# Kernel optimization log

Hardware: AMD Instinct MI355X
Metric: run time of the kernel (lower is better)

Reference implementation:

```python
import jax, jax.numpy as jnp
import numpy as np

DIM = 1024
N_HEADS = 16
HEAD_DIM = DIM // N_HEADS


def setup_inputs() -> dict:
    key = jax.random.key(0)
    ks = jax.random.split(key, 5)
    x = jax.random.normal(ks[0], (2, 2048, DIM), dtype=jnp.float32)
    # nn.Linear-style init scale
    s = 1.0 / np.sqrt(DIM)
    W_qkv = jax.random.uniform(ks[1], (DIM, 3 * DIM), jnp.float32, -s, s)
    b_qkv = jax.random.uniform(ks[2], (3 * DIM,), jnp.float32, -s, s)
    W_proj = jax.random.uniform(ks[3], (DIM, DIM), jnp.float32, -s, s)
    b_proj = jax.random.uniform(ks[4], (DIM,), jnp.float32, -s, s)
    return {"x": x, "W_qkv": W_qkv, "b_qkv": b_qkv, "W_proj": W_proj, "b_proj": b_proj}


def reference(x, W_qkv, b_qkv, W_proj, b_proj):
    B, S, D = x.shape
    scale = HEAD_DIM ** -0.5
    qkv = x @ W_qkv + b_qkv                                   # [B,S,3D]
    qkv = qkv.reshape(B, S, 3, N_HEADS, HEAD_DIM)
    q = qkv[:, :, 0].transpose(0, 2, 1, 3)                    # [B,H,S,d]
    k = qkv[:, :, 1].transpose(0, 2, 1, 3)
    v = qkv[:, :, 2].transpose(0, 2, 1, 3)
    attn = jnp.einsum('bhqd,bhkd->bhqk', q, k) * scale        # [B,H,S,S]
    attn = jax.nn.softmax(attn, axis=-1)
    out = jnp.einsum('bhqk,bhkd->bhqd', attn, v)              # [B,H,S,d]
    out = out.transpose(0, 2, 1, 3).reshape(B, S, D)
    return out @ W_proj + b_proj
```

## Files before the change

### kernel.cpp

```cpp
#include <hip/hip_runtime.h>
#include <stdint.h>

typedef unsigned short u16;
typedef __attribute__((ext_vector_type(8))) short bf16x8;
typedef __attribute__((ext_vector_type(4))) float f32x4;
typedef __attribute__((ext_vector_type(16))) float f32x16;
typedef __attribute__((ext_vector_type(4))) u16 us4;
typedef __attribute__((ext_vector_type(8))) u16 us8;

__device__ __forceinline__ u16 f2bf(float f) {
  union { float f; unsigned u; } v; v.f = f;
  unsigned r = v.u + 0x7fffu + ((v.u >> 16) & 1u);
  return (u16)(r >> 16);
}

__device__ __forceinline__ float bf2f(u16 b) {
  union { float f; unsigned u; } v; v.u = ((unsigned)b) << 16;
  return v.f;
}

__device__ __forceinline__ unsigned cvtpk(float a, float b) {
  unsigned r;
  asm("v_cvt_pk_bf16_f32 %0, %1, %2" : "=v"(r) : "v"(a), "v"(b));
  return r;
}

__device__ __forceinline__ float fast_exp2(float x) {
#if __has_builtin(__builtin_amdgcn_exp2f)
  return __builtin_amdgcn_exp2f(x);
#else
  return exp2f(x);
#endif
}

__device__ __forceinline__ void gld16(const void* g, void* l) {
  __builtin_amdgcn_global_load_lds(
      (const __attribute__((address_space(1))) void*)g,
      (__attribute__((address_space(3))) void*)l, 16, 0, 0);
}

__global__ void prep_kernel(const float* __restrict__ x, u16* __restrict__ Xb,
                            const float* __restrict__ Wqkv, u16* __restrict__ Wqkt,
                            const float* __restrict__ Wproj, u16* __restrict__ Wpt) {
  __shared__ u16 tile[32][33];
  const int blk = blockIdx.x;
  if (blk < 4096) {
    const int i = blk * 256 + threadIdx.x;
    f32x4 v = ((const f32x4*)x)[i];
    us4 r;
#pragma unroll
    for (int j = 0; j < 4; ++j) r[j] = f2bf(v[j]);
    ((us4*)Xb)[i] = r;
    return;
  }
  const float* in;
  u16* out;
  int R, C, t;
  if (blk < 7168) { in = Wqkv; out = Wqkt; R = 1024; C = 3072; t = blk - 4096; }
  else            { in = Wproj; out = Wpt; R = 1024; C = 1024; t = blk - 7168; }
  const int gx = (C == 3072) ? (t % 96) : (t % 32);
  const int gy = (C == 3072) ? (t / 96) : (t / 32);
  const int tx = threadIdx.x & 31, ty = threadIdx.x >> 5;
  const int c0 = gx * 32, r0 = gy * 32;
#pragma unroll
  for (int j = 0; j < 4; ++j)
    tile[ty + j * 8][tx] = f2bf(in[(size_t)(r0 + ty + j * 8) * C + c0 + tx]);
  __syncthreads();
#pragma unroll
  for (int j = 0; j < 4; ++j)
    out[(size_t)(c0 + ty + j * 8) * R + r0 + tx] = tile[tx][ty + j * 8];
}

__global__ __launch_bounds__(256) void qkv_gemm_kernel(
    const u16* __restrict__ A, const u16* __restrict__ Bt, const float* __restrict__ bias,
    u16* __restrict__ Qb, u16* __restrict__ Kb, u16* __restrict__ Vtb) {
  __shared__ u16 sm[17408];
  u16* As = sm;
  u16* Bs = sm + 4096;
  const int tid = threadIdx.x;
  const int w = tid >> 6, l = tid & 63, quad = l >> 4, lanelo = l & 15;
  const int wr = w >> 1, wc = w & 1;
  const int flat = blockIdx.x + 32 * blockIdx.y;
  const int xcd = flat & 7, lid = flat >> 3;
  const long m0 = (long)((xcd >> 1) * 8 + (lid & 7)) * 128;
  const long n0 = (long)((xcd & 1) * 12 + (lid >> 3)) * 128;

  f32x4 acc[4][4];
#pragma unroll
  for (int i = 0; i < 4; ++i)
#pragma unroll
    for (int j = 0; j < 4; ++j) acc[i][j] = (f32x4){0.f, 0.f, 0.f, 0.f};

  const u16* ag = A + (m0 + w * 32 + (l >> 2)) * 1024 + (l & 3) * 8;
  const u16* bg = Bt + (n0 + w * 32 + (l >> 2)) * 1024 + (l & 3) * 8;
  u16* asl = As + w * 1024;
  u16* bsl = Bs + w * 1024;

  for (int kt = 0; kt < 32; ++kt) {
    const int ko = kt * 32;
    gld16(ag + ko, asl);
    gld16(ag + 16 * 1024 + ko, asl + 512);
    gld16(bg + ko, bsl);
    gld16(bg + 16 * 1024 + ko, bsl + 512);
    __syncthreads();
    bf16x8 af[4], bf[4];
#pragma unroll
    for (int mt = 0; mt < 4; ++mt)
      af[mt] = *(const bf16x8*)(As + (wr * 64 + mt * 16 + lanelo) * 32 + quad * 8);
#pragma unroll
    for (int nt = 0; nt < 4; ++nt)
      bf[nt] = *(const bf16x8*)(Bs + (wc * 64 + nt * 16 + lanelo) * 32 + quad * 8);
#pragma unroll
    for (int mt = 0; mt < 4; ++mt)
#pragma unroll
      for (int nt = 0; nt < 4; ++nt)
        acc[mt][nt] = __builtin_amdgcn_mfma_f32_16x16x32_bf16(af[mt], bf[nt], acc[mt][nt], 0, 0, 0);
    __syncthreads();
  }

  const int t = (int)(n0 >> 10);
  const float scl = (t == 0) ? 0.18033688011112042f : 1.0f;

  float bias_v[4];
#pragma unroll
  for (int nt = 0; nt < 4; ++nt) bias_v[nt] = bias[n0 + wc * 64 + nt * 16 + lanelo];

  u16* Ct = sm;
#pragma unroll
  for (int mt = 0; mt < 4; ++mt)
#pragma unroll
    for (int nt = 0; nt < 4; ++nt)
#pragma unroll
      for (int r = 0; r < 4; ++r)
        Ct[(wr * 64 + mt * 16 + quad * 4 + r) * 136 + wc * 64 + nt * 16 + lanelo] =
            f2bf((acc[mt][nt][r] + bias_v[nt]) * scl);
  __syncthreads();

  const int b = (int)(m0 >> 11);
  const int s0 = (int)(m0 & 2047);
  const int h0 = (int)((n0 & 1023) >> 6);

  if (t < 2) {
    u16* dst = (t == 0) ? Qb : Kb;
#pragma unroll
    for (int p = 0; p < 8; ++p) {
      const int hh = p >> 2;
      const int sl = (p & 3) * 32 + (tid >> 3);
      const int c8 = tid & 7;
      us8 v = *(const us8*)(Ct + sl * 136 + hh * 64 + c8 * 8);
      const int pos = (c8 + sl) & 7;
      const size_t off = ((size_t)((b * 16 + h0 + hh) * 2048 + s0 + sl)) * 64 + pos * 8;
      *(us8*)(dst + off) = v;
    }
  } else {
#pragma unroll
    for (int p = 0; p < 8; ++p) {
      const int hh = p >> 2;
      const int dl = (p & 3) * 16 + (tid >> 4);
      const int c16 = tid & 15;
      us8 v;
#pragma unroll
      for (int j = 0; j < 8; ++j) v[j] = Ct[(c16 * 8 + j) * 136 + hh * 64 + dl];
      const int pos = (c16 + dl) & 15;
      const size_t off = ((size_t)((b * 16 + h0 + hh) * 64 + dl)) * 2048 + s0 + pos * 8;
      *(us8*)(Vtb + off) = v;
    }
  }
}

__global__ __launch_bounds__(512, 4) void attn_kernel(
    const u16* __restrict__ Qb, const u16* __restrict__ Kb,
    const u16* __restrict__ Vtb, u16* __restrict__ Ob) {
  __shared__ u16 Ks[2][2][4096];
  __shared__ u16 Vs[2][2][4096];
  const int tid = threadIdx.x;
  const int w8 = tid >> 6;
  const int z = w8 >> 2, w = w8 & 3;
  const int l = tid & 63;
  const int m = l & 31, hi = l >> 5;
  const int fid = blockIdx.x;
  const int head = (fid & 7) + 8 * ((fid >> 3) & 3);
  const int qt = fid >> 5;
  const u16* Qh = Qb + (size_t)head * 2048 * 64;
  const u16* Kh = Kb + (size_t)head * 2048 * 64;
  const u16* Vh = Vtb + (size_t)head * 64 * 2048;
  const int permaddr = (l ^ 32) << 2;

  const int qrow = qt * 128 + w * 32 + m;
  bf16x8 qf[4];
#pragma unroll
  for (int ks = 0; ks < 4; ++ks) {
    const int pos = (ks * 2 + hi + qrow) & 7;
    qf[ks] = *(const bf16x8*)(Qh + (size_t)qrow * 64 + pos * 8);
  }

  f32x16 o0, o1;
#pragma unroll
  for (int i = 0; i < 16; ++i) { o0[i] = 0.f; o1[i] = 0.f; }
  float sp[4] = {0.f, 0.f, 0.f, 0.f};

  auto stage = [&](int kb, int buf) {
    const u16* kbase = Kh + (size_t)kb * 4096;
#pragma unroll
    for (int j = 0; j < 2; ++j) {
      const int i = w * 2 + j;
      gld16(kbase + i * 512 + l * 8, &Ks[z][buf][i * 512]);
    }
    const int panel = kb >> 1, half = kb & 1;
#pragma unroll
    for (int j = 0; j < 2; ++j) {
      const int i = w * 2 + j;
      const int dd = i * 8 + (l >> 3);
      const int p = l & 7;
      const int q = (p - dd) & 7;
      const int pos16 = (half * 8 + q + dd) & 15;
      gld16(Vh + (size_t)dd * 2048 + panel * 128 + pos16 * 8,
            &Vs[z][buf][i * 512]);
    }
  };

  int cur = 0;
  stage(z * 16, 0);

  for (int kt = 0; kt < 16; ++kt) {
    __builtin_amdgcn_s_barrier();
    if (kt < 15) {
      stage(z * 16 + kt + 1, cur ^ 1);
      asm volatile("s_waitcnt vmcnt(4)" ::: "memory");
    } else {
      asm volatile("s_waitcnt vmcnt(0)" ::: "memory");
    }
    __builtin_amdgcn_s_barrier();

#pragma unroll
    for (int g = 0; g < 2; ++g) {
      f32x16 st;
#pragma unroll
      for (int i = 0; i < 16; ++i) st[i] = 0.f;
      const int key = g * 32 + m;
#pragma unroll
      for (int ks = 0; ks < 4; ++ks) {
        const int pos = (ks * 2 + hi + key) & 7;
        bf16x8 kf = *(const bf16x8*)(&Ks[z][cur][key * 64 + pos * 8]);
        st = __builtin_amdgcn_mfma_f32_32x32x16_bf16(kf, qf[ks], st, 0, 0, 0);
      }

      float p[16];
#pragma unroll
      for (int r = 0; r < 16; ++r) p[r] = fast_exp2(st[r]);
#pragma unroll
      for (int r = 0; r < 16; ++r) sp[r & 3] += p[r];

      unsigned W[8];
#pragma unroll
      for (int i = 0; i < 8; ++i) W[i] = cvtpk(p[2 * i], p[2 * i + 1]);

#pragma unroll
      for (int s = 0; s < 2; ++s) {
        unsigned w0 = W[4 * s], w1 = W[4 * s + 1];
        unsigned w2 = W[4 * s + 2], w3 = W[4 * s + 3];
        asm("v_permlane32_swap_b32 %0, %1" : "+v"(w0), "+v"(w2));
        asm("v_permlane32_swap_b32 %0, %1" : "+v"(w1), "+v"(w3));
        int4 fd;
        fd.x = (int)w0;
        fd.y = (int)w1;
        fd.z = (int)w2;
        fd.w = (int)w3;
        union { int4 i; bf16x8 v; } pu; pu.i = fd;
        const int c = g * 4 + s * 2 + hi;
#pragma unroll
        for (int n = 0; n < 2; ++n) {
          const int d = n * 32 + m;
          const int pos = (c + d) & 7;
          bf16x8 vf = *(const bf16x8*)(&Vs[z][cur][d * 64 + pos * 8]);
          if (n == 0) o0 = __builtin_amdgcn_mfma_f32_32x32x16_bf16(pu.v, vf, o0, 0, 0, 0);
          else        o1 = __builtin_amdgcn_mfma_f32_32x32x16_bf16(pu.v, vf, o1, 0, 0, 0);
        }
      }
    }
    cur ^= 1;
  }
  __syncthreads();

  const float sacc = (sp[0] + sp[1]) + (sp[2] + sp[3]);

  union { float f; int i; } sv; sv.f = sacc;
  union { float f; int i; } pv; pv.i = __builtin_amdgcn_ds_bpermute(permaddr, sv.i);
  const float ltot = sacc + pv.f;

  float* Osl = (float*)Ks;
  float* Lz1 = (float*)Vs;

  if (z == 1) {
    if (hi == 0) Lz1[w * 32 + m] = ltot;
#pragma unroll
    for (int r = 0; r < 16; ++r) {
      const int qlocal = (r & 3) + 8 * (r >> 2) + 4 * hi;
      Osl[w * 2048 + qlocal * 64 + m] = o0[r];
      Osl[w * 2048 + qlocal * 64 + 32 + m] = o1[r];
    }
  }
  __syncthreads();
  if (z == 0) {
    const float lfull = ltot + Lz1[w * 32 + m];
    union { float f; int i; } li; li.f = 1.0f / lfull;
    const int b = head >> 4, h = head & 15;
#pragma unroll
    for (int r = 0; r < 16; ++r) {
      const int qlocal = (r & 3) + 8 * (r >> 2) + 4 * hi;
      union { float f; int i; } lg;
      lg.i = __builtin_amdgcn_ds_bpermute(qlocal << 2, li.i);
      const float v0 = (o0[r] + Osl[w * 2048 + qlocal * 64 + m]) * lg.f;
      const float v1 = (o1[r] + Osl[w * 2048 + qlocal * 64 + 32 + m]) * lg.f;
      const size_t base =
          ((size_t)(b * 2048 + qt * 128 + w * 32 + qlocal)) * 1024 + h * 64;
      Ob[base + m] = f2bf(v0);
      Ob[base + 32 + m] = f2bf(v1);
    }
  }
}

__global__ __launch_bounds__(256) void proj_gemm_kernel(
    const u16* __restrict__ A, const u16* __restrict__ Bt,
    const float* __restrict__ bias, float* __restrict__ out) {
  __shared__ u16 sm[6144];
  u16* As = sm;
  u16* Bs = sm + 4096;
  const int tid = threadIdx.x;
  const int w = tid >> 6, l = tid & 63, quad = l >> 4, lanelo = l & 15;
  const int wr = w >> 1, wc = w & 1;
  const int flat = blockIdx.x + 32 * blockIdx.y;
  const int xcd = flat & 7, lid = flat >> 3;
  const long m0 = (long)(xcd * 4 + (lid & 3)) * 128;
  const long n0 = (long)(lid >> 2) * 64;

  f32x4 acc[4][2];
#pragma unroll
  for (int i = 0; i < 4; ++i)
#pragma unroll
    for (int j = 0; j < 2; ++j) acc[i][j] = (f32x4){0.f, 0.f, 0.f, 0.f};

  const u16* ag = A + (m0 + w * 32 + (l >> 2)) * 1024 + (l & 3) * 8;
  const u16* bg = Bt + (n0 + w * 16 + (l >> 2)) * 1024 + (l & 3) * 8;
  u16* asl = As + w * 1024;
  u16* bsl = Bs + w * 512;

  for (int kt = 0; kt < 32; ++kt) {
    const int ko = kt * 32;
    gld16(ag + ko, asl);
    gld16(ag + 16 * 1024 + ko, asl + 512);
    gld16(bg + ko, bsl);
    __syncthreads();
    bf16x8 af[4], bf[2];
#pragma unroll
    for (int mt = 0; mt < 4; ++mt)
      af[mt] = *(const bf16x8*)(As + (wr * 64 + mt * 16 + lanelo) * 32 + quad * 8);
#pragma unroll
    for (int nt = 0; nt < 2; ++nt)
      bf[nt] = *(const bf16x8*)(Bs + (wc * 32 + nt * 16 + lanelo) * 32 + quad * 8);
#pragma unroll
    for (int mt = 0; mt < 4; ++mt)
#pragma unroll
      for (int nt = 0; nt < 2; ++nt)
        acc[mt][nt] = __builtin_amdgcn_mfma_f32_16x16x32_bf16(af[mt], bf[nt], acc[mt][nt], 0, 0, 0);
    __syncthreads();
  }

  float bias_v[2];
#pragma unroll
  for (int nt = 0; nt < 2; ++nt)
    bias_v[nt] = bias[n0 + wc * 32 + nt * 16 + lanelo];

#pragma unroll
  for (int mt = 0; mt < 4; ++mt)
#pragma unroll
    for (int nt = 0; nt < 2; ++nt)
#pragma unroll
      for (int r = 0; r < 4; ++r) {
        const size_t mm = m0 + wr * 64 + mt * 16 + quad * 4 + r;
        const size_t nn = n0 + wc * 32 + nt * 16 + lanelo;
        out[mm * 1024 + nn] = acc[mt][nt][r] + bias_v[nt];
      }
}

extern "C" void kernel_launch(void* const* d_in, const int* in_sizes, int n_in,
                              void* d_out, int out_size, void* d_ws, size_t ws_size,
                              hipStream_t stream) {
  const float* x = (const float*)d_in[0];
  const float* Wqkv = (const float*)d_in[1];
  const float* bqkv = (const float*)d_in[2];
  const float* Wproj = (const float*)d_in[3];
  const float* bproj = (const float*)d_in[4];
  float* out = (float*)d_out;
  char* ws = (char*)d_ws;

  u16* Xb   = (u16*)(ws);
  u16* Ob   = (u16*)(ws);
  u16* Wqkt = (u16*)(ws + 8388608);
  u16* Qb   = (u16*)(ws + 16777216);
  u16* Kb   = (u16*)(ws + 25165824);
  u16* Vtb  = (u16*)(ws + 33554432);
  u16* Wpt  = (u16*)(ws + 41943040);

  prep_kernel<<<8192, 256, 0, stream>>>(x, Xb, Wqkv, Wqkt, Wproj, Wpt);
  qkv_gemm_kernel<<<dim3(32, 24), 256, 0, stream>>>(Xb, Wqkt, bqkv, Qb, Kb, Vtb);
  attn_kernel<<<512, 512, 0, stream>>>(Qb, Kb, Vtb, Ob);
  proj_gemm_kernel<<<dim3(32, 16), 256, 0, stream>>>(Ob, Wpt, bproj, out);
}
```

Before: 184.0 us.

## Compute softmax row sums via MFMA, widen weight transpose tiles, add setprio

The attention kernel now accumulates the softmax denominator with an extra MFMA against a ones vector instead of scalar adds and cross-lane permutes. It also raises wave priority around the MFMA blocks and precomputes the K/V staging offsets. Separately, the weight transpose in the prep kernel now uses 64x32 tiles with vectorized 16-byte stores and fewer blocks. These changes trade extra matrix-core work for fewer VALU and LDS-permute operations, and aim to make the transposes more bandwidth-efficient.

```diff
diff --git a/kernel.cpp b/kernel.cpp
--- a/kernel.cpp
+++ b/kernel.cpp
@@ -14,11 +14,6 @@
   return (u16)(r >> 16);
 }
 
-__device__ __forceinline__ float bf2f(u16 b) {
-  union { float f; unsigned u; } v; v.u = ((unsigned)b) << 16;
-  return v.f;
-}
-
 __device__ __forceinline__ unsigned cvtpk(float a, float b) {
   unsigned r;
   asm("v_cvt_pk_bf16_f32 %0, %1, %2" : "=v"(r) : "v"(a), "v"(b));
@@ -42,7 +37,7 @@
 __global__ void prep_kernel(const float* __restrict__ x, u16* __restrict__ Xb,
                             const float* __restrict__ Wqkv, u16* __restrict__ Wqkt,
                             const float* __restrict__ Wproj, u16* __restrict__ Wpt) {
-  __shared__ u16 tile[32][33];
+  __shared__ u16 tile[64][33];
   const int blk = blockIdx.x;
   if (blk < 4096) {
     const int i = blk * 256 + threadIdx.x;
@@ -55,20 +50,23 @@
   }
   const float* in;
   u16* out;
-  int R, C, t;
-  if (blk < 7168) { in = Wqkv; out = Wqkt; R = 1024; C = 3072; t = blk - 4096; }
-  else            { in = Wproj; out = Wpt; R = 1024; C = 1024; t = blk - 7168; }
+  int C, t;
+  if (blk < 5632) { in = Wqkv; out = Wqkt; C = 3072; t = blk - 4096; }
+  else            { in = Wproj; out = Wpt; C = 1024; t = blk - 5632; }
+  const int R = 1024;
   const int gx = (C == 3072) ? (t % 96) : (t % 32);
   const int gy = (C == 3072) ? (t / 96) : (t / 32);
   const int tx = threadIdx.x & 31, ty = threadIdx.x >> 5;
-  const int c0 = gx * 32, r0 = gy * 32;
-#pragma unroll
-  for (int j = 0; j < 4; ++j)
+  const int c0 = gx * 32, r0 = gy * 64;
+#pragma unroll
+  for (int j = 0; j < 8; ++j)
     tile[ty + j * 8][tx] = f2bf(in[(size_t)(r0 + ty + j * 8) * C + c0 + tx]);
   __syncthreads();
-#pragma unroll
-  for (int j = 0; j < 4; ++j)
-    out[(size_t)(c0 + ty + j * 8) * R + r0 + tx] = tile[tx][ty + j * 8];
+  const int oc = threadIdx.x >> 3, ob = (threadIdx.x & 7) * 8;
+  us8 o;
+#pragma unroll
+  for (int k = 0; k < 8; ++k) o[k] = tile[ob + k][oc];
+  *(us8*)(&out[(size_t)(c0 + oc) * R + r0 + ob]) = o;
 }
 
 __global__ __launch_bounds__(256) void qkv_gemm_kernel(
@@ -184,7 +182,6 @@
   const u16* Qh = Qb + (size_t)head * 2048 * 64;
   const u16* Kh = Kb + (size_t)head * 2048 * 64;
   const u16* Vh = Vtb + (size_t)head * 64 * 2048;
-  const int permaddr = (l ^ 32) << 2;
 
   const int qrow = qt * 128 + w * 32 + m;
   bf16x8 qf[4];
@@ -194,29 +191,33 @@
     qf[ks] = *(const bf16x8*)(Qh + (size_t)qrow * 64 + pos * 8);
   }
 
-  f32x16 o0, o1;
-#pragma unroll
-  for (int i = 0; i < 16; ++i) { o0[i] = 0.f; o1[i] = 0.f; }
-  float sp[4] = {0.f, 0.f, 0.f, 0.f};
+  bf16x8 onesB;
+#pragma unroll
+  for (int i = 0; i < 8; ++i) onesB[i] = (short)0x3F80;
+
+  f32x16 o0, o1, sl;
+#pragma unroll
+  for (int i = 0; i < 16; ++i) { o0[i] = 0.f; o1[i] = 0.f; sl[i] = 0.f; }
+
+  const int i0 = w * 2, i1 = w * 2 + 1;
+  const size_t kOff0 = (size_t)i0 * 512 + l * 8;
+  const size_t kOff1 = (size_t)i1 * 512 + l * 8;
+  const int dd0 = i0 * 8 + (l >> 3), dd1 = i1 * 8 + (l >> 3);
+  const int p_ = l & 7;
+  const int q0 = (p_ - dd0) & 7, q1 = (p_ - dd1) & 7;
+  const size_t vE0 = (size_t)dd0 * 2048 + (size_t)(((q0 + dd0) & 15)) * 8;
+  const size_t vO0 = (size_t)dd0 * 2048 + (size_t)(((8 + q0 + dd0) & 15)) * 8;
+  const size_t vE1 = (size_t)dd1 * 2048 + (size_t)(((q1 + dd1) & 15)) * 8;
+  const size_t vO1 = (size_t)dd1 * 2048 + (size_t)(((8 + q1 + dd1) & 15)) * 8;
 
   auto stage = [&](int kb, int buf) {
-    const u16* kbase = Kh + (size_t)kb * 4096;
-#pragma unroll
-    for (int j = 0; j < 2; ++j) {
-      const int i = w * 2 + j;
-      gld16(kbase + i * 512 + l * 8, &Ks[z][buf][i * 512]);
-    }
-    const int panel = kb >> 1, half = kb & 1;
-#pragma unroll
-    for (int j = 0; j < 2; ++j) {
-      const int i = w * 2 + j;
-      const int dd = i * 8 + (l >> 3);
-      const int p = l & 7;
-      const int q = (p - dd) & 7;
-      const int pos16 = (half * 8 + q + dd) & 15;
-      gld16(Vh + (size_t)dd * 2048 + panel * 128 + pos16 * 8,
-            &Vs[z][buf][i * 512]);
-    }
+    const u16* kp = Kh + (size_t)kb * 4096;
+    gld16(kp + kOff0, &Ks[z][buf][i0 * 512]);
+    gld16(kp + kOff1, &Ks[z][buf][i1 * 512]);
+    const u16* vp = Vh + (size_t)(kb >> 1) * 128;
+    const int odd = kb & 1;
+    gld16(vp + (odd ? vO0 : vE0), &Vs[z][buf][i0 * 512]);
+    gld16(vp + (odd ? vO1 : vE1), &Vs[z][buf][i1 * 512]);
   };
 
   int cur = 0;
@@ -238,18 +239,18 @@
 #pragma unroll
       for (int i = 0; i < 16; ++i) st[i] = 0.f;
       const int key = g * 32 + m;
+      __builtin_amdgcn_s_setprio(1);
 #pragma unroll
       for (int ks = 0; ks < 4; ++ks) {
         const int pos = (ks * 2 + hi + key) & 7;
         bf16x8 kf = *(const bf16x8*)(&Ks[z][cur][key * 64 + pos * 8]);
         st = __builtin_amdgcn_mfma_f32_32x32x16_bf16(kf, qf[ks], st, 0, 0, 0);
       }
+      __builtin_amdgcn_s_setprio(0);
 
       float p[16];
 #pragma unroll
       for (int r = 0; r < 16; ++r) p[r] = fast_exp2(st[r]);
-#pragma unroll
-      for (int r = 0; r < 16; ++r) sp[r & 3] += p[r];
 
       unsigned W[8];
 #pragma unroll
@@ -268,6 +269,8 @@
         fd.w = (int)w3;
         union { int4 i; bf16x8 v; } pu; pu.i = fd;
         const int c = g * 4 + s * 2 + hi;
+        __builtin_amdgcn_s_setprio(1);
+        sl = __builtin_amdgcn_mfma_f32_32x32x16_bf16(pu.v, onesB, sl, 0, 0, 0);
 #pragma unroll
         for (int n = 0; n < 2; ++n) {
           const int d = n * 32 + m;
@@ -276,23 +279,24 @@
           if (n == 0) o0 = __builtin_amdgcn_mfma_f32_32x32x16_bf16(pu.v, vf, o0, 0, 0, 0);
           else        o1 = __builtin_amdgcn_mfma_f32_32x32x16_bf16(pu.v, vf, o1, 0, 0, 0);
         }
+        __builtin_amdgcn_s_setprio(0);
       }
     }
     cur ^= 1;
   }
   __syncthreads();
-
-  const float sacc = (sp[0] + sp[1]) + (sp[2] + sp[3]);
-
-  union { float f; int i; } sv; sv.f = sacc;
-  union { float f; int i; } pv; pv.i = __builtin_amdgcn_ds_bpermute(permaddr, sv.i);
-  const float ltot = sacc + pv.f;
 
   float* Osl = (float*)Ks;
   float* Lz1 = (float*)Vs;
 
   if (z == 1) {
-    if (hi == 0) Lz1[w * 32 + m] = ltot;
+    if (m == 0) {
+#pragma unroll
+      for (int r = 0; r < 16; ++r) {
+        const int qlocal = (r & 3) + 8 * (r >> 2) + 4 * hi;
+        Lz1[w * 32 + qlocal] = sl[r];
+      }
+    }
 #pragma unroll
     for (int r = 0; r < 16; ++r) {
       const int qlocal = (r & 3) + 8 * (r >> 2) + 4 * hi;
@@ -302,16 +306,14 @@
   }
   __syncthreads();
   if (z == 0) {
-    const float lfull = ltot + Lz1[w * 32 + m];
-    union { float f; int i; } li; li.f = 1.0f / lfull;
     const int b = head >> 4, h = head & 15;
 #pragma unroll
     for (int r = 0; r < 16; ++r) {
       const int qlocal = (r & 3) + 8 * (r >> 2) + 4 * hi;
-      union { float f; int i; } lg;
-      lg.i = __builtin_amdgcn_ds_bpermute(qlocal << 2, li.i);
-      const float v0 = (o0[r] + Osl[w * 2048 + qlocal * 64 + m]) * lg.f;
-      const float v1 = (o1[r] + Osl[w * 2048 + qlocal * 64 + 32 + m]) * lg.f;
+      const float lfull = sl[r] + Lz1[w * 32 + qlocal];
+      const float inv = 1.0f / lfull;
+      const float v0 = (o0[r] + Osl[w * 2048 + qlocal * 64 + m]) * inv;
+      const float v1 = (o1[r] + Osl[w * 2048 + qlocal * 64 + 32 + m]) * inv;
       const size_t base =
           ((size_t)(b * 2048 + qt * 128 + w * 32 + qlocal)) * 1024 + h * 64;
       Ob[base + m] = f2bf(v0);
@@ -402,7 +404,7 @@
   u16* Vtb  = (u16*)(ws + 33554432);
   u16* Wpt  = (u16*)(ws + 41943040);
 
-  prep_kernel<<<8192, 256, 0, stream>>>(x, Xb, Wqkv, Wqkt, Wproj, Wpt);
+  prep_kernel<<<6144, 256, 0, stream>>>(x, Xb, Wqkv, Wqkt, Wproj, Wpt);
   qkv_gemm_kernel<<<dim3(32, 24), 256, 0, stream>>>(Xb, Wqkt, bqkv, Qb, Kb, Vtb);
   attn_kernel<<<512, 512, 0, stream>>>(Qb, Kb, Vtb, Ob);
   proj_gemm_kernel<<<dim3(32, 16), 256, 0, stream>>>(Ob, Wpt, bproj, out);
```

After: 183.0 us. About the same (-0.5%).
